# Kernel optimization log

Measured on AMD Instinct MI355X. Metric: run time of the kernel, lower is better.

The kernel has to match this reference:

```python
import jax, jax.numpy as jnp
import numpy as np

V, E, H, Z, T = 8185, 353, 191, 13, 25
START = 19


def _lstm(x, h, c, k, rk, b):
    # Keras LSTMCell: gates ordered i, f, g(candidate), o
    gates = x @ k + h @ rk + b                      # (B, 4H)
    i, f, g, o = jnp.split(gates, 4, axis=-1)
    c_new = jax.nn.sigmoid(f) * c + jax.nn.sigmoid(i) * jnp.tanh(g)
    h_new = jax.nn.sigmoid(o) * jnp.tanh(c_new)
    return h_new, c_new


def setup_inputs() -> dict:
    key = jax.random.key(0)
    ks = jax.random.split(key, 18)
    B = 256
    s = 0.05
    inp = {
        "inputs": jax.random.randint(ks[0], (B, T), 0, V),
        "epsilon": jax.random.normal(ks[1], (Z,), jnp.float32),
        "emb": jax.random.normal(ks[2], (V, E), jnp.float32) * s,
        "inf_k": jax.random.normal(ks[3], (E, 4 * H), jnp.float32) * s,
        "inf_rk": jax.random.normal(ks[4], (H, 4 * H), jnp.float32) * s,
        "inf_b": jnp.zeros((4 * H,), jnp.float32),
        "mu_w": jax.random.normal(ks[5], (H, Z), jnp.float32) * s,
        "mu_b": jnp.zeros((Z,), jnp.float32),
        "sig_w": jax.random.normal(ks[6], (H, Z), jnp.float32) * s,
        "sig_b": jnp.zeros((Z,), jnp.float32),
        "init_w": jax.random.normal(ks[7], (Z, H), jnp.float32) * s,
        "init_b": jnp.zeros((H,), jnp.float32),
        "gen_k": jax.random.normal(ks[8], (E, 4 * H), jnp.float32) * s,
        "gen_rk": jax.random.normal(ks[9], (H, 4 * H), jnp.float32) * s,
        "gen_b": jnp.zeros((4 * H,), jnp.float32),
        "out_w": jax.random.normal(ks[10], (H, V), jnp.float32) * s,
        "out_b": jnp.zeros((V,), jnp.float32),
    }
    return inp


def reference(inputs, epsilon, emb, inf_k, inf_rk, inf_b, mu_w, mu_b,
              sig_w, sig_b, init_w, init_b, gen_k, gen_rk, gen_b,
              out_w, out_b):
    B = inputs.shape[0]
    # ----- encoder (inference LSTM over the full sequence) -----
    inf_emb = emb[inputs]                             # (B, T, E)

    def enc_step(carry, x_t):
        h, c = carry
        h, c = _lstm(x_t, h, c, inf_k, inf_rk, inf_b)
        return (h, c), None

    h0 = jnp.zeros((B, H), emb.dtype)
    (h_enc, _), _ = jax.lax.scan(enc_step, (h0, h0),
                                 jnp.swapaxes(inf_emb, 0, 1))  # scan over T

    mu = h_enc @ mu_w + mu_b                          # (B, Z)
    sigma = h_enc @ sig_w + sig_b                     # (B, Z)
    z = mu + epsilon * sigma                          # shared epsilon (Z,)

    init_state = z @ init_w + init_b                  # (B, H)
    emb0 = jnp.broadcast_to(emb[START], (B, E))       # start token embedding

    def dec_step(carry, _):
        h, c, x = carry
        h, c = _lstm(x, h, c, gen_k, gen_rk, gen_b)
        logits = h @ out_w + out_b                    # (B, V)
        new_ind = jnp.argmax(logits, axis=-1)         # (B,)
        x_next = emb[new_ind]                         # (B, E)
        return (h, c, x_next), logits

    _, logits_seq = jax.lax.scan(dec_step, (init_state, init_state, emb0),
                                 None, length=T)      # (T, B, V)
    return jnp.swapaxes(logits_seq, 0, 1)             # (B, T, V)
```

## Files before the change

kernel.cpp:

```cpp
#include <hip/hip_runtime.h>
#include <math.h>

#define V_  8185
#define E_  353
#define H_  191
#define FH_ 764
#define Z_  13
#define T_  25
#define START_ 19
#define VP_ 8192
#define NT_ 32

__device__ __forceinline__ float sigf(float x) { return 1.0f / (1.0f + expf(-x)); }

__global__ __launch_bounds__(256) void pad_w_kernel(const float* __restrict__ src,
                                                    float* __restrict__ dst) {
  int i = blockIdx.x * 256 + threadIdx.x;
  if (i >= H_ * VP_) return;
  int k = i >> 13;
  int j = i & (VP_ - 1);
  dst[i] = (j < V_) ? src[(size_t)k * V_ + j] : 0.0f;
}

__global__ __launch_bounds__(256) void gemm_ew(const float* __restrict__ emb,
                                               const float* __restrict__ W,
                                               float* __restrict__ C, int M,
                                               const int* __restrict__ inputs,
                                               int mode, int B) {
  __shared__ __align__(16) float AT[E_ * 16];
  const int tid = threadIdx.x;
  const int n0 = blockIdx.x * 256;
  const int m0 = blockIdx.y * 16;
  for (int i = tid; i < 16 * E_; i += 256) {
    int r = i / E_, k = i - r * E_;
    int m = m0 + r;
    float v = 0.0f;
    if (m < M) {
      int row;
      if (mode == 0) row = m;
      else { int t = m / B, b = m - t * B; row = inputs[b * T_ + t]; }
      v = emb[(size_t)row * E_ + k];
    }
    AT[k * 16 + r] = v;
  }
  __syncthreads();
  const int lane = tid & 63;
  const int w4 = (tid >> 6) * 4;
  const int j = n0 + lane * 4;
  if (j >= FH_) return;
  float4 c0 = {0,0,0,0}, c1 = {0,0,0,0}, c2 = {0,0,0,0}, c3 = {0,0,0,0};
  const float* wc = W + j;
  const float* at = AT + w4;
  for (int k = 0; k < E_; ++k) {
    float4 wv = *(const float4*)(wc + (size_t)k * FH_);
    float4 a  = *(const float4*)(at + k * 16);
    c0.x = fmaf(a.x, wv.x, c0.x); c0.y = fmaf(a.x, wv.y, c0.y);
    c0.z = fmaf(a.x, wv.z, c0.z); c0.w = fmaf(a.x, wv.w, c0.w);
    c1.x = fmaf(a.y, wv.x, c1.x); c1.y = fmaf(a.y, wv.y, c1.y);
    c1.z = fmaf(a.y, wv.z, c1.z); c1.w = fmaf(a.y, wv.w, c1.w);
    c2.x = fmaf(a.z, wv.x, c2.x); c2.y = fmaf(a.z, wv.y, c2.y);
    c2.z = fmaf(a.z, wv.z, c2.z); c2.w = fmaf(a.z, wv.w, c2.w);
    c3.x = fmaf(a.w, wv.x, c3.x); c3.y = fmaf(a.w, wv.y, c3.y);
    c3.z = fmaf(a.w, wv.z, c3.z); c3.w = fmaf(a.w, wv.w, c3.w);
  }
  const int mb = m0 + w4;
  if (mb + 0 < M) *(float4*)(C + (size_t)(mb + 0) * FH_ + j) = c0;
  if (mb + 1 < M) *(float4*)(C + (size_t)(mb + 1) * FH_ + j) = c1;
  if (mb + 2 < M) *(float4*)(C + (size_t)(mb + 2) * FH_ + j) = c2;
  if (mb + 3 < M) *(float4*)(C + (size_t)(mb + 3) * FH_ + j) = c3;
}

__global__ __launch_bounds__(256) void lstm_step(const float* __restrict__ xk,
                                                 const float* __restrict__ rk,
                                                 const float* __restrict__ bias,
                                                 const float* __restrict__ h_in,
                                                 const float* __restrict__ c_in,
                                                 float* __restrict__ h_out,
                                                 float* __restrict__ c_out,
                                                 const float* __restrict__ pmax,
                                                 const int* __restrict__ pidx,
                                                 int mode, int first) {
  __shared__ float hs[16 * H_];
  __shared__ float xs[16 * 32];
  __shared__ float bs[32];
  __shared__ int   tk[16];
  __shared__ float pv[16 * NT_];
  __shared__ int   pi[16 * NT_];
  __shared__ float gb[32 * 16];

  const int tid = threadIdx.x;
  const int c0 = blockIdx.x * 8;
  const int m0 = blockIdx.y * 16;

  if (mode) {
    if (first) {
      if (tid < 16) tk[tid] = START_;
    } else {
      for (int i = tid; i < 16 * NT_; i += 256) {
        int row = i >> 5, s = i & (NT_ - 1);
        pv[i] = pmax[(size_t)(m0 + row) * NT_ + s];
        pi[i] = pidx[(size_t)(m0 + row) * NT_ + s];
      }
      __syncthreads();
      if (tid < 16) {
        float bv = pv[tid * NT_]; int bi = pi[tid * NT_];
        for (int s = 1; s < NT_; ++s) {
          float v = pv[tid * NT_ + s]; int ii = pi[tid * NT_ + s];
          if (v > bv || (v == bv && ii < bi)) { bv = v; bi = ii; }
        }
        tk[tid] = bi;
      }
    }
    __syncthreads();
  }

  for (int i = tid; i < 16 * H_; i += 256) hs[i] = h_in[(size_t)m0 * H_ + i];
  for (int i = tid; i < 16 * 32; i += 256) {
    int row = i >> 5, q = i & 31;
    int jj = c0 + (q & 7);
    int jg = jj + H_ * (q >> 3);
    float xv = 0.0f;
    if (jj < H_) {
      const float* xrow = mode ? (xk + (size_t)tk[row] * FH_)
                               : (xk + (size_t)(m0 + row) * FH_);
      xv = xrow[jg];
    }
    xs[i] = xv;
  }
  if (tid < 32) {
    int jj = c0 + (tid & 7);
    bs[tid] = (jj < H_) ? bias[jj + H_ * (tid >> 3)] : 0.0f;
  }
  __syncthreads();

  const int q = tid & 31, rg = tid >> 5;
  const int jj = c0 + (q & 7);
  const int jg = jj + H_ * (q >> 3);
  float a0 = 0.0f, a1 = 0.0f;
  if (jj < H_) {
    const float* rkp = rk + jg;
    const float* h0p = hs + rg * H_;
    const float* h1p = hs + (rg + 8) * H_;
    for (int k = 0; k < H_; ++k) {
      float wv = rkp[(size_t)k * FH_];
      a0 = fmaf(h0p[k], wv, a0);
      a1 = fmaf(h1p[k], wv, a1);
    }
  }
  gb[q * 16 + rg] = a0;
  gb[q * 16 + rg + 8] = a1;
  __syncthreads();

  if (tid < 128) {
    int cc = tid & 7, row = tid >> 3;
    int jc = c0 + cc;
    if (jc < H_) {
      float gi = gb[(cc      ) * 16 + row] + xs[row * 32 + cc      ] + bs[cc];
      float gf = gb[( 8 + cc ) * 16 + row] + xs[row * 32 +  8 + cc ] + bs[ 8 + cc];
      float gg = gb[(16 + cc ) * 16 + row] + xs[row * 32 + 16 + cc ] + bs[16 + cc];
      float go = gb[(24 + cc ) * 16 + row] + xs[row * 32 + 24 + cc ] + bs[24 + cc];
      float co = c_in[(size_t)(m0 + row) * H_ + jc];
      float cn = sigf(gf) * co + sigf(gi) * tanhf(gg);
      float hn = sigf(go) * tanhf(cn);
      c_out[(size_t)(m0 + row) * H_ + jc] = cn;
      h_out[(size_t)(m0 + row) * H_ + jc] = hn;
    }
  }
}

__global__ __launch_bounds__(256) void logits_argmax(const float* __restrict__ h,
                                                     const float* __restrict__ wp,
                                                     const float* __restrict__ ob,
                                                     float* __restrict__ out, int t,
                                                     float* __restrict__ pmax,
                                                     int* __restrict__ pidx) {
  __shared__ __align__(16) float AT[H_ * 16];
  const int tid = threadIdx.x;
  const int n0 = blockIdx.x * 256;
  const int m0 = blockIdx.y * 16;
  for (int i = tid; i < 16 * H_; i += 256) {
    int r = i / H_, k = i - r * H_;
    AT[k * 16 + r] = h[(size_t)m0 * H_ + i];
  }
  __syncthreads();
  const int lane = tid & 63;
  const int w4 = (tid >> 6) * 4;
  const int j = n0 + lane * 4;
  float4 c0 = {0,0,0,0}, c1 = {0,0,0,0}, c2 = {0,0,0,0}, c3 = {0,0,0,0};
  const float* wc = wp + j;
  const float* at = AT + w4;
  for (int k = 0; k < H_; ++k) {
    float4 wv = *(const float4*)(wc + (size_t)k * VP_);
    float4 a  = *(const float4*)(at + k * 16);
    c0.x = fmaf(a.x, wv.x, c0.x); c0.y = fmaf(a.x, wv.y, c0.y);
    c0.z = fmaf(a.x, wv.z, c0.z); c0.w = fmaf(a.x, wv.w, c0.w);
    c1.x = fmaf(a.y, wv.x, c1.x); c1.y = fmaf(a.y, wv.y, c1.y);
    c1.z = fmaf(a.y, wv.z, c1.z); c1.w = fmaf(a.y, wv.w, c1.w);
    c2.x = fmaf(a.z, wv.x, c2.x); c2.y = fmaf(a.z, wv.y, c2.y);
    c2.z = fmaf(a.z, wv.z, c2.z); c2.w = fmaf(a.z, wv.w, c2.w);
    c3.x = fmaf(a.w, wv.x, c3.x); c3.y = fmaf(a.w, wv.y, c3.y);
    c3.z = fmaf(a.w, wv.z, c3.z); c3.w = fmaf(a.w, wv.w, c3.w);
  }
  float bias[4];
#pragma unroll
  for (int u = 0; u < 4; ++u) bias[u] = (j + u < V_) ? ob[j + u] : 0.0f;
  float4 accs[4] = {c0, c1, c2, c3};
  const int b0 = m0 + w4;
#pragma unroll
  for (int r = 0; r < 4; ++r) {
    const int b = b0 + r;
    float v[4] = {accs[r].x + bias[0], accs[r].y + bias[1],
                  accs[r].z + bias[2], accs[r].w + bias[3]};
    float* orow = out + ((size_t)b * T_ + t) * V_ + j;
#pragma unroll
    for (int u = 0; u < 4; ++u)
      if (j + u < V_) orow[u] = v[u];
    float bv = -INFINITY; int bi = 0;
#pragma unroll
    for (int u = 0; u < 4; ++u)
      if (j + u < V_ && v[u] > bv) { bv = v[u]; bi = j + u; }
#pragma unroll
    for (int off = 1; off < 64; off <<= 1) {
      float ov = __shfl_xor(bv, off, 64);
      int   oi = __shfl_xor(bi, off, 64);
      if (ov > bv || (ov == bv && oi < bi)) { bv = ov; bi = oi; }
    }
    if (lane == 0) {
      pmax[(size_t)b * NT_ + blockIdx.x] = bv;
      pidx[(size_t)b * NT_ + blockIdx.x] = bi;
    }
  }
}

__global__ __launch_bounds__(64) void latent_k(const float* __restrict__ h,
                                               const float* __restrict__ eps,
                                               const float* __restrict__ mu_w,
                                               const float* __restrict__ mu_b,
                                               const float* __restrict__ sig_w,
                                               const float* __restrict__ sig_b,
                                               const float* __restrict__ iw,
                                               const float* __restrict__ ib,
                                               float* __restrict__ h0,
                                               float* __restrict__ c0) {
  __shared__ float zs[4 * Z_];
  const int tid = threadIdx.x;
  const int m0 = blockIdx.x * 4;
  if (tid < 4 * Z_) {
    int row = tid / Z_, qz = tid - row * Z_;
    const float* hr = h + (size_t)(m0 + row) * H_;
    float mu = mu_b[qz], sg = sig_b[qz];
    for (int k = 0; k < H_; ++k) {
      float hv = hr[k];
      mu = fmaf(hv, mu_w[k * Z_ + qz], mu);
      sg = fmaf(hv, sig_w[k * Z_ + qz], sg);
    }
    zs[tid] = mu + eps[qz] * sg;
  }
  __syncthreads();
  for (int i = tid; i < 4 * H_; i += 64) {
    int row = i / H_, col = i - row * H_;
    float acc = ib[col];
#pragma unroll
    for (int qz = 0; qz < Z_; ++qz)
      acc = fmaf(zs[row * Z_ + qz], iw[qz * H_ + col], acc);
    h0[(size_t)(m0 + row) * H_ + col] = acc;
    c0[(size_t)(m0 + row) * H_ + col] = acc;
  }
}

extern "C" void kernel_launch(void* const* d_in, const int* in_sizes, int n_in,
                              void* d_out, int out_size, void* d_ws, size_t ws_size,
                              hipStream_t stream) {
  const int*   inputs = (const int*)  d_in[0];
  const float* eps    = (const float*)d_in[1];
  const float* emb    = (const float*)d_in[2];
  const float* inf_k  = (const float*)d_in[3];
  const float* inf_rk = (const float*)d_in[4];
  const float* inf_b  = (const float*)d_in[5];
  const float* mu_w   = (const float*)d_in[6];
  const float* mu_b   = (const float*)d_in[7];
  const float* sig_w  = (const float*)d_in[8];
  const float* sig_b  = (const float*)d_in[9];
  const float* init_w = (const float*)d_in[10];
  const float* init_b = (const float*)d_in[11];
  const float* gen_k  = (const float*)d_in[12];
  const float* gen_rk = (const float*)d_in[13];
  const float* gen_b  = (const float*)d_in[14];
  const float* out_w  = (const float*)d_in[15];
  const float* out_b  = (const float*)d_in[16];
  float* out = (float*)d_out;

  const int B = in_sizes[0] / T_;
  const int BH = B * H_;

  float* ws = (float*)d_ws;
  size_t off = 0;
  float* EK = ws + off; off += (size_t)V_ * FH_;
  float* XK = ws + off; off += (size_t)T_ * B * FH_;
  float* WP = ws + off; off += (size_t)H_ * VP_;
  float* hbase = ws + off; off += (size_t)8 * BH;
  float* he[2] = {hbase + 0 * BH, hbase + 2 * BH};
  float* ce[2] = {hbase + 1 * BH, hbase + 3 * BH};
  float* hd[2] = {hbase + 4 * BH, hbase + 6 * BH};
  float* cd[2] = {hbase + 5 * BH, hbase + 7 * BH};
  float* pmax = ws + off; off += (size_t)B * NT_;
  int*   pidx = (int*)(ws + off); off += (size_t)B * NT_;

  hipMemsetAsync(hbase, 0, (size_t)2 * BH * sizeof(float), stream);

  pad_w_kernel<<<(H_ * VP_ + 255) / 256, 256, 0, stream>>>(out_w, WP);
  gemm_ew<<<dim3(3, (V_ + 15) / 16), 256, 0, stream>>>(emb, gen_k, EK, V_, nullptr, 0, B);
  gemm_ew<<<dim3(3, (T_ * B) / 16), 256, 0, stream>>>(emb, inf_k, XK, T_ * B, inputs, 1, B);

  for (int t = 0; t < T_; ++t) {
    lstm_step<<<dim3(24, B / 16), 256, 0, stream>>>(
        XK + (size_t)t * B * FH_, inf_rk, inf_b,
        he[t & 1], ce[t & 1], he[(t + 1) & 1], ce[(t + 1) & 1],
        nullptr, nullptr, 0, 0);
  }

  latent_k<<<B / 4, 64, 0, stream>>>(he[T_ & 1], eps, mu_w, mu_b, sig_w, sig_b,
                                     init_w, init_b, hd[0], cd[0]);

  for (int t = 0; t < T_; ++t) {
    lstm_step<<<dim3(24, B / 16), 256, 0, stream>>>(
        EK, gen_rk, gen_b,
        hd[t & 1], cd[t & 1], hd[(t + 1) & 1], cd[(t + 1) & 1],
        pmax, pidx, 1, (t == 0) ? 1 : 0);
    logits_argmax<<<dim3(NT_, B / 16), 256, 0, stream>>>(
        hd[(t + 1) & 1], WP, out_b, out, t, pmax, pidx);
  }
}
```

Measured before the change: 1.890 ms.

## Fuse all stages into one persistent kernel with per-row-group grid barriers

Replaces the roughly 80 separate kernel launches (pad, two GEMMs, 25 encoder steps, latent, 25 decoder lstm+logits pairs) with a single persistent kernel of 512 blocks. Blocks synchronise through atomic-counter barriers: one grid-wide barrier after the precompute, then barriers scoped to each 16-row batch group for the recurrent steps. The argmax is reduced with a 64-bit packed atomicMax key instead of per-tile partial buffers and a second reduction. This targets launch and inter-kernel gap overhead, at the cost of relying on all 512 blocks being co-resident (spin-barrier deadlock risk otherwise) and of idle blocks during the LSTM phases.

```diff
diff --git a/kernel.cpp b/kernel.cpp
--- a/kernel.cpp
+++ b/kernel.cpp
@@ -9,28 +9,52 @@
 #define T_  25
 #define START_ 19
 #define VP_ 8192
-#define NT_ 32
+#define NB_ 512
 
 __device__ __forceinline__ float sigf(float x) { return 1.0f / (1.0f + expf(-x)); }
 
-__global__ __launch_bounds__(256) void pad_w_kernel(const float* __restrict__ src,
-                                                    float* __restrict__ dst) {
-  int i = blockIdx.x * 256 + threadIdx.x;
-  if (i >= H_ * VP_) return;
-  int k = i >> 13;
-  int j = i & (VP_ - 1);
-  dst[i] = (j < V_) ? src[(size_t)k * V_ + j] : 0.0f;
-}
-
-__global__ __launch_bounds__(256) void gemm_ew(const float* __restrict__ emb,
-                                               const float* __restrict__ W,
-                                               float* __restrict__ C, int M,
-                                               const int* __restrict__ inputs,
-                                               int mode, int B) {
-  __shared__ __align__(16) float AT[E_ * 16];
-  const int tid = threadIdx.x;
-  const int n0 = blockIdx.x * 256;
-  const int m0 = blockIdx.y * 16;
+union SMem {
+  float AT_g[16 * E_];
+  struct {
+    float hs[16 * H_];
+    float xs[16 * 32];
+    float bs[32];
+    float gb[32 * 16];
+    int   tk[16];
+  } l;
+  float AT_l[16 * H_];
+  float zs[16 * Z_];
+};
+
+__device__ __forceinline__ void bar_sync(unsigned* bar, unsigned members) {
+  __syncthreads();
+  if (threadIdx.x == 0) {
+    unsigned g = __hip_atomic_load(bar + 1, __ATOMIC_RELAXED, __HIP_MEMORY_SCOPE_AGENT);
+    unsigned a = __hip_atomic_fetch_add(bar, 1u, __ATOMIC_ACQ_REL, __HIP_MEMORY_SCOPE_AGENT);
+    if (a == members - 1) {
+      __hip_atomic_store(bar, 0u, __ATOMIC_RELAXED, __HIP_MEMORY_SCOPE_AGENT);
+      __hip_atomic_fetch_add(bar + 1, 1u, __ATOMIC_RELEASE, __HIP_MEMORY_SCOPE_AGENT);
+    } else {
+      while (__hip_atomic_load(bar + 1, __ATOMIC_ACQUIRE, __HIP_MEMORY_SCOPE_AGENT) == g)
+        __builtin_amdgcn_s_sleep(4);
+    }
+  }
+  __syncthreads();
+}
+
+__device__ __forceinline__ unsigned long long pack_key(float v, int idx) {
+  unsigned u = __float_as_uint(v);
+  u = (u & 0x80000000u) ? ~u : (u | 0x80000000u);
+  return ((unsigned long long)u << 32) | (unsigned)(0x7FFFFFFFu - idx);
+}
+
+__device__ void gemm_tile(const float* __restrict__ emb, const float* __restrict__ W,
+                          float* __restrict__ C, int M, int ct, int m0,
+                          const int* __restrict__ inputs, int mode, int B,
+                          float* AT) {
+  const int tid = threadIdx.x;
+  const int n0 = ct * 256;
+  __syncthreads();
   for (int i = tid; i < 16 * E_; i += 256) {
     int r = i / E_, k = i - r * E_;
     int m = m0 + r;
@@ -38,7 +62,7 @@
     if (m < M) {
       int row;
       if (mode == 0) row = m;
-      else { int t = m / B, b = m - t * B; row = inputs[b * T_ + t]; }
+      else { int t = m / B, bb = m - t * B; row = inputs[bb * T_ + t]; }
       v = emb[(size_t)row * E_ + k];
     }
     AT[k * 16 + r] = v;
@@ -47,118 +71,97 @@
   const int lane = tid & 63;
   const int w4 = (tid >> 6) * 4;
   const int j = n0 + lane * 4;
-  if (j >= FH_) return;
-  float4 c0 = {0,0,0,0}, c1 = {0,0,0,0}, c2 = {0,0,0,0}, c3 = {0,0,0,0};
-  const float* wc = W + j;
-  const float* at = AT + w4;
-  for (int k = 0; k < E_; ++k) {
-    float4 wv = *(const float4*)(wc + (size_t)k * FH_);
-    float4 a  = *(const float4*)(at + k * 16);
-    c0.x = fmaf(a.x, wv.x, c0.x); c0.y = fmaf(a.x, wv.y, c0.y);
-    c0.z = fmaf(a.x, wv.z, c0.z); c0.w = fmaf(a.x, wv.w, c0.w);
-    c1.x = fmaf(a.y, wv.x, c1.x); c1.y = fmaf(a.y, wv.y, c1.y);
-    c1.z = fmaf(a.y, wv.z, c1.z); c1.w = fmaf(a.y, wv.w, c1.w);
-    c2.x = fmaf(a.z, wv.x, c2.x); c2.y = fmaf(a.z, wv.y, c2.y);
-    c2.z = fmaf(a.z, wv.z, c2.z); c2.w = fmaf(a.z, wv.w, c2.w);
-    c3.x = fmaf(a.w, wv.x, c3.x); c3.y = fmaf(a.w, wv.y, c3.y);
-    c3.z = fmaf(a.w, wv.z, c3.z); c3.w = fmaf(a.w, wv.w, c3.w);
-  }
-  const int mb = m0 + w4;
-  if (mb + 0 < M) *(float4*)(C + (size_t)(mb + 0) * FH_ + j) = c0;
-  if (mb + 1 < M) *(float4*)(C + (size_t)(mb + 1) * FH_ + j) = c1;
-  if (mb + 2 < M) *(float4*)(C + (size_t)(mb + 2) * FH_ + j) = c2;
-  if (mb + 3 < M) *(float4*)(C + (size_t)(mb + 3) * FH_ + j) = c3;
-}
-
-__global__ __launch_bounds__(256) void lstm_step(const float* __restrict__ xk,
-                                                 const float* __restrict__ rk,
-                                                 const float* __restrict__ bias,
-                                                 const float* __restrict__ h_in,
-                                                 const float* __restrict__ c_in,
-                                                 float* __restrict__ h_out,
-                                                 float* __restrict__ c_out,
-                                                 const float* __restrict__ pmax,
-                                                 const int* __restrict__ pidx,
-                                                 int mode, int first) {
-  __shared__ float hs[16 * H_];
-  __shared__ float xs[16 * 32];
-  __shared__ float bs[32];
-  __shared__ int   tk[16];
-  __shared__ float pv[16 * NT_];
-  __shared__ int   pi[16 * NT_];
-  __shared__ float gb[32 * 16];
-
-  const int tid = threadIdx.x;
-  const int c0 = blockIdx.x * 8;
-  const int m0 = blockIdx.y * 16;
-
-  if (mode) {
-    if (first) {
-      if (tid < 16) tk[tid] = START_;
-    } else {
-      for (int i = tid; i < 16 * NT_; i += 256) {
-        int row = i >> 5, s = i & (NT_ - 1);
-        pv[i] = pmax[(size_t)(m0 + row) * NT_ + s];
-        pi[i] = pidx[(size_t)(m0 + row) * NT_ + s];
+  if (j < FH_) {
+    float4 c0 = {0,0,0,0}, c1 = {0,0,0,0}, c2 = {0,0,0,0}, c3 = {0,0,0,0};
+    const float* wc = W + j;
+    const float* at = AT + w4;
+    for (int k = 0; k < E_; ++k) {
+      float4 wv = *(const float4*)(wc + (size_t)k * FH_);
+      float4 a  = *(const float4*)(at + k * 16);
+      c0.x = fmaf(a.x, wv.x, c0.x); c0.y = fmaf(a.x, wv.y, c0.y);
+      c0.z = fmaf(a.x, wv.z, c0.z); c0.w = fmaf(a.x, wv.w, c0.w);
+      c1.x = fmaf(a.y, wv.x, c1.x); c1.y = fmaf(a.y, wv.y, c1.y);
+      c1.z = fmaf(a.y, wv.z, c1.z); c1.w = fmaf(a.y, wv.w, c1.w);
+      c2.x = fmaf(a.z, wv.x, c2.x); c2.y = fmaf(a.z, wv.y, c2.y);
+      c2.z = fmaf(a.z, wv.z, c2.z); c2.w = fmaf(a.z, wv.w, c2.w);
+      c3.x = fmaf(a.w, wv.x, c3.x); c3.y = fmaf(a.w, wv.y, c3.y);
+      c3.z = fmaf(a.w, wv.z, c3.z); c3.w = fmaf(a.w, wv.w, c3.w);
+    }
+    const int mb = m0 + w4;
+    if (mb + 0 < M) *(float4*)(C + (size_t)(mb + 0) * FH_ + j) = c0;
+    if (mb + 1 < M) *(float4*)(C + (size_t)(mb + 1) * FH_ + j) = c1;
+    if (mb + 2 < M) *(float4*)(C + (size_t)(mb + 2) * FH_ + j) = c2;
+    if (mb + 3 < M) *(float4*)(C + (size_t)(mb + 3) * FH_ + j) = c3;
+  }
+}
+
+template <int MODE>
+__device__ void lstm_dev(const float* __restrict__ xk, const float* __restrict__ rk,
+                         const float* __restrict__ bias,
+                         const float* __restrict__ h_in, const float* __restrict__ c_in,
+                         float* __restrict__ h_out, float* __restrict__ c_out,
+                         const unsigned long long* __restrict__ tok_prev,
+                         int cb, int m0, SMem& sm) {
+  const int tid = threadIdx.x;
+  const int c0 = cb * 8;
+
+  if (MODE) {
+    if (tid < 16) {
+      int tkn = START_;
+      if (tok_prev) {
+        unsigned long long key = tok_prev[m0 + tid];
+        tkn = (int)(0x7FFFFFFFu - (unsigned)(key & 0xFFFFFFFFu));
       }
-      __syncthreads();
-      if (tid < 16) {
-        float bv = pv[tid * NT_]; int bi = pi[tid * NT_];
-        for (int s = 1; s < NT_; ++s) {
-          float v = pv[tid * NT_ + s]; int ii = pi[tid * NT_ + s];
-          if (v > bv || (v == bv && ii < bi)) { bv = v; bi = ii; }
-        }
-        tk[tid] = bi;
-      }
+      sm.l.tk[tid] = tkn;
     }
     __syncthreads();
   }
 
-  for (int i = tid; i < 16 * H_; i += 256) hs[i] = h_in[(size_t)m0 * H_ + i];
+  for (int i = tid; i < 16 * H_; i += 256) sm.l.hs[i] = h_in[(size_t)m0 * H_ + i];
   for (int i = tid; i < 16 * 32; i += 256) {
     int row = i >> 5, q = i & 31;
     int jj = c0 + (q & 7);
     int jg = jj + H_ * (q >> 3);
     float xv = 0.0f;
     if (jj < H_) {
-      const float* xrow = mode ? (xk + (size_t)tk[row] * FH_)
+      const float* xrow = MODE ? (xk + (size_t)sm.l.tk[row] * FH_)
                                : (xk + (size_t)(m0 + row) * FH_);
       xv = xrow[jg];
     }
-    xs[i] = xv;
+    sm.l.xs[i] = xv;
   }
   if (tid < 32) {
     int jj = c0 + (tid & 7);
-    bs[tid] = (jj < H_) ? bias[jj + H_ * (tid >> 3)] : 0.0f;
-  }
-  __syncthreads();
-
-  const int q = tid & 31, rg = tid >> 5;
+    sm.l.bs[tid] = (jj < H_) ? bias[jj + H_ * (tid >> 3)] : 0.0f;
+  }
+  __syncthreads();
+
+  const int q = tid & 31, rgi = tid >> 5;
   const int jj = c0 + (q & 7);
   const int jg = jj + H_ * (q >> 3);
   float a0 = 0.0f, a1 = 0.0f;
   if (jj < H_) {
     const float* rkp = rk + jg;
-    const float* h0p = hs + rg * H_;
-    const float* h1p = hs + (rg + 8) * H_;
+    const float* h0p = sm.l.hs + rgi * H_;
+    const float* h1p = sm.l.hs + (rgi + 8) * H_;
     for (int k = 0; k < H_; ++k) {
       float wv = rkp[(size_t)k * FH_];
       a0 = fmaf(h0p[k], wv, a0);
       a1 = fmaf(h1p[k], wv, a1);
     }
   }
-  gb[q * 16 + rg] = a0;
-  gb[q * 16 + rg + 8] = a1;
+  sm.l.gb[q * 16 + rgi] = a0;
+  sm.l.gb[q * 16 + rgi + 8] = a1;
   __syncthreads();
 
   if (tid < 128) {
     int cc = tid & 7, row = tid >> 3;
     int jc = c0 + cc;
     if (jc < H_) {
-      float gi = gb[(cc      ) * 16 + row] + xs[row * 32 + cc      ] + bs[cc];
-      float gf = gb[( 8 + cc ) * 16 + row] + xs[row * 32 +  8 + cc ] + bs[ 8 + cc];
-      float gg = gb[(16 + cc ) * 16 + row] + xs[row * 32 + 16 + cc ] + bs[16 + cc];
-      float go = gb[(24 + cc ) * 16 + row] + xs[row * 32 + 24 + cc ] + bs[24 + cc];
+      float gi = sm.l.gb[(cc     ) * 16 + row] + sm.l.xs[row * 32 + cc     ] + sm.l.bs[cc];
+      float gf = sm.l.gb[( 8 + cc) * 16 + row] + sm.l.xs[row * 32 +  8 + cc] + sm.l.bs[ 8 + cc];
+      float gg = sm.l.gb[(16 + cc) * 16 + row] + sm.l.xs[row * 32 + 16 + cc] + sm.l.bs[16 + cc];
+      float go = sm.l.gb[(24 + cc) * 16 + row] + sm.l.xs[row * 32 + 24 + cc] + sm.l.bs[24 + cc];
       float co = c_in[(size_t)(m0 + row) * H_ + jc];
       float cn = sigf(gf) * co + sigf(gi) * tanhf(gg);
       float hn = sigf(go) * tanhf(cn);
@@ -168,16 +171,12 @@
   }
 }
 
-__global__ __launch_bounds__(256) void logits_argmax(const float* __restrict__ h,
-                                                     const float* __restrict__ wp,
-                                                     const float* __restrict__ ob,
-                                                     float* __restrict__ out, int t,
-                                                     float* __restrict__ pmax,
-                                                     int* __restrict__ pidx) {
-  __shared__ __align__(16) float AT[H_ * 16];
-  const int tid = threadIdx.x;
-  const int n0 = blockIdx.x * 256;
-  const int m0 = blockIdx.y * 16;
+__device__ void logits_dev(const float* __restrict__ h, const float* __restrict__ wp,
+                           const float* __restrict__ ob, float* __restrict__ out,
+                           int t, unsigned long long* __restrict__ tok_cur,
+                           int ct, int m0, float* AT) {
+  const int tid = threadIdx.x;
+  const int n0 = ct * 256;
   for (int i = tid; i < 16 * H_; i += 256) {
     int r = i / H_, k = i - r * H_;
     AT[k * 16 + r] = h[(size_t)m0 * H_ + i];
@@ -225,27 +224,18 @@
       int   oi = __shfl_xor(bi, off, 64);
       if (ov > bv || (ov == bv && oi < bi)) { bv = ov; bi = oi; }
     }
-    if (lane == 0) {
-      pmax[(size_t)b * NT_ + blockIdx.x] = bv;
-      pidx[(size_t)b * NT_ + blockIdx.x] = bi;
-    }
-  }
-}
-
-__global__ __launch_bounds__(64) void latent_k(const float* __restrict__ h,
-                                               const float* __restrict__ eps,
-                                               const float* __restrict__ mu_w,
-                                               const float* __restrict__ mu_b,
-                                               const float* __restrict__ sig_w,
-                                               const float* __restrict__ sig_b,
-                                               const float* __restrict__ iw,
-                                               const float* __restrict__ ib,
-                                               float* __restrict__ h0,
-                                               float* __restrict__ c0) {
-  __shared__ float zs[4 * Z_];
-  const int tid = threadIdx.x;
-  const int m0 = blockIdx.x * 4;
-  if (tid < 4 * Z_) {
+    if (lane == 0) atomicMax(tok_cur + b, pack_key(bv, bi));
+  }
+}
+
+__device__ void latent_dev(const float* __restrict__ h, const float* __restrict__ eps,
+                           const float* __restrict__ mu_w, const float* __restrict__ mu_b,
+                           const float* __restrict__ sig_w, const float* __restrict__ sig_b,
+                           const float* __restrict__ iw, const float* __restrict__ ib,
+                           float* __restrict__ h0, float* __restrict__ c0,
+                           int m0, SMem& sm) {
+  const int tid = threadIdx.x;
+  if (tid < 16 * Z_) {
     int row = tid / Z_, qz = tid - row * Z_;
     const float* hr = h + (size_t)(m0 + row) * H_;
     float mu = mu_b[qz], sg = sig_b[qz];
@@ -254,17 +244,87 @@
       mu = fmaf(hv, mu_w[k * Z_ + qz], mu);
       sg = fmaf(hv, sig_w[k * Z_ + qz], sg);
     }
-    zs[tid] = mu + eps[qz] * sg;
-  }
-  __syncthreads();
-  for (int i = tid; i < 4 * H_; i += 64) {
+    sm.zs[tid] = mu + eps[qz] * sg;
+  }
+  __syncthreads();
+  for (int i = tid; i < 16 * H_; i += 256) {
     int row = i / H_, col = i - row * H_;
     float acc = ib[col];
 #pragma unroll
     for (int qz = 0; qz < Z_; ++qz)
-      acc = fmaf(zs[row * Z_ + qz], iw[qz * H_ + col], acc);
+      acc = fmaf(sm.zs[row * Z_ + qz], iw[qz * H_ + col], acc);
     h0[(size_t)(m0 + row) * H_ + col] = acc;
     c0[(size_t)(m0 + row) * H_ + col] = acc;
+  }
+}
+
+__global__ __launch_bounds__(256, 2) void mega(
+    const int* __restrict__ inputs, const float* __restrict__ eps,
+    const float* __restrict__ emb,
+    const float* __restrict__ inf_k, const float* __restrict__ inf_rk,
+    const float* __restrict__ inf_b,
+    const float* __restrict__ mu_w, const float* __restrict__ mu_b,
+    const float* __restrict__ sig_w, const float* __restrict__ sig_b,
+    const float* __restrict__ init_w, const float* __restrict__ init_b,
+    const float* __restrict__ gen_k, const float* __restrict__ gen_rk,
+    const float* __restrict__ gen_b,
+    const float* __restrict__ out_w, const float* __restrict__ out_b,
+    float* __restrict__ out,
+    float* __restrict__ EK, float* __restrict__ XK, float* __restrict__ WP,
+    float* __restrict__ hbase, unsigned long long* __restrict__ tok,
+    unsigned* __restrict__ bars, int B) {
+  __shared__ SMem sm;
+  const int b = blockIdx.x;
+  const int tid = threadIdx.x;
+  const int rg = b >> 5;
+  const int ct = b & 31;
+  const int m0 = rg * 16;
+  const int BH = B * H_;
+  unsigned* dbar = bars + rg * 32;
+  unsigned* gbar = bars + 16 * 32;
+
+  float* he[2] = {hbase,          hbase + 2 * BH};
+  float* ce[2] = {hbase + BH,     hbase + 3 * BH};
+  float* hd[2] = {hbase + 4 * BH, hbase + 6 * BH};
+  float* cd[2] = {hbase + 5 * BH, hbase + 7 * BH};
+
+  for (int i = b * 256 + tid; i < H_ * VP_; i += NB_ * 256) {
+    int k = i >> 13, j = i & (VP_ - 1);
+    WP[i] = (j < V_) ? out_w[(size_t)k * V_ + j] : 0.0f;
+  }
+  for (int s = 0; s < 3; ++s) {
+    int tt = b + NB_ * s;
+    gemm_tile(emb, gen_k, EK, V_, tt % 3, (tt / 3) * 16, nullptr, 0, B, sm.AT_g);
+  }
+  for (int s = 0; s < 3; ++s) {
+    int tt = b + NB_ * s;
+    if (tt < 1200)
+      gemm_tile(emb, inf_k, XK, T_ * B, tt % 3, (tt / 3) * 16, inputs, 1, B, sm.AT_g);
+  }
+  bar_sync(gbar, NB_);
+
+  for (int t = 0; t < T_; ++t) {
+    if (ct < 24)
+      lstm_dev<0>(XK + (size_t)t * B * FH_, inf_rk, inf_b,
+                  he[t & 1], ce[t & 1], he[(t + 1) & 1], ce[(t + 1) & 1],
+                  nullptr, ct, m0, sm);
+    bar_sync(dbar, 32);
+  }
+
+  if (ct == 0)
+    latent_dev(he[T_ & 1], eps, mu_w, mu_b, sig_w, sig_b, init_w, init_b,
+               hd[0], cd[0], m0, sm);
+  bar_sync(dbar, 32);
+
+  for (int t = 0; t < T_; ++t) {
+    if (ct < 24)
+      lstm_dev<1>(EK, gen_rk, gen_b,
+                  hd[t & 1], cd[t & 1], hd[(t + 1) & 1], cd[(t + 1) & 1],
+                  t ? (tok + (size_t)(t - 1) * B) : nullptr, ct, m0, sm);
+    bar_sync(dbar, 32);
+    logits_dev(hd[(t + 1) & 1], WP, out_b, out, t, tok + (size_t)t * B,
+               ct, m0, sm.AT_l);
+    bar_sync(dbar, 32);
   }
 }
 
@@ -295,39 +355,18 @@
 
   float* ws = (float*)d_ws;
   size_t off = 0;
-  float* EK = ws + off; off += (size_t)V_ * FH_;
-  float* XK = ws + off; off += (size_t)T_ * B * FH_;
-  float* WP = ws + off; off += (size_t)H_ * VP_;
-  float* hbase = ws + off; off += (size_t)8 * BH;
-  float* he[2] = {hbase + 0 * BH, hbase + 2 * BH};
-  float* ce[2] = {hbase + 1 * BH, hbase + 3 * BH};
-  float* hd[2] = {hbase + 4 * BH, hbase + 6 * BH};
-  float* cd[2] = {hbase + 5 * BH, hbase + 7 * BH};
-  float* pmax = ws + off; off += (size_t)B * NT_;
-  int*   pidx = (int*)(ws + off); off += (size_t)B * NT_;
-
-  hipMemsetAsync(hbase, 0, (size_t)2 * BH * sizeof(float), stream);
-
-  pad_w_kernel<<<(H_ * VP_ + 255) / 256, 256, 0, stream>>>(out_w, WP);
-  gemm_ew<<<dim3(3, (V_ + 15) / 16), 256, 0, stream>>>(emb, gen_k, EK, V_, nullptr, 0, B);
-  gemm_ew<<<dim3(3, (T_ * B) / 16), 256, 0, stream>>>(emb, inf_k, XK, T_ * B, inputs, 1, B);
-
-  for (int t = 0; t < T_; ++t) {
-    lstm_step<<<dim3(24, B / 16), 256, 0, stream>>>(
-        XK + (size_t)t * B * FH_, inf_rk, inf_b,
-        he[t & 1], ce[t & 1], he[(t + 1) & 1], ce[(t + 1) & 1],
-        nullptr, nullptr, 0, 0);
-  }
-
-  latent_k<<<B / 4, 64, 0, stream>>>(he[T_ & 1], eps, mu_w, mu_b, sig_w, sig_b,
-                                     init_w, init_b, hd[0], cd[0]);
-
-  for (int t = 0; t < T_; ++t) {
-    lstm_step<<<dim3(24, B / 16), 256, 0, stream>>>(
-        EK, gen_rk, gen_b,
-        hd[t & 1], cd[t & 1], hd[(t + 1) & 1], cd[(t + 1) & 1],
-        pmax, pidx, 1, (t == 0) ? 1 : 0);
-    logits_argmax<<<dim3(NT_, B / 16), 256, 0, stream>>>(
-        hd[(t + 1) & 1], WP, out_b, out, t, pmax, pidx);
-  }
-}
+  float* hbase = ws + off;                         off += (size_t)8 * BH;
+  unsigned long long* tok = (unsigned long long*)(ws + off); off += (size_t)T_ * B * 2;
+  unsigned* bars = (unsigned*)(ws + off);          off += 1024;
+  size_t zero_bytes = off * sizeof(float);
+  float* EK = ws + off;                            off += (size_t)V_ * FH_;
+  float* XK = ws + off;                            off += (size_t)T_ * B * FH_;
+  float* WP = ws + off;                            off += (size_t)H_ * VP_;
+
+  hipMemsetAsync(ws, 0, zero_bytes, stream);
+
+  mega<<<NB_, 256, 0, stream>>>(inputs, eps, emb, inf_k, inf_rk, inf_b,
+                                mu_w, mu_b, sig_w, sig_b, init_w, init_b,
+                                gen_k, gen_rk, gen_b, out_w, out_b, out,
+                                EK, XK, WP, hbase, tok, bars, B);
+}
```

After: 6.117 ms. 3.24x slower.
